# Performance work log

Hardware: AMD Instinct MI355X
Metric: run time of the kernel (lower is better)

## Reference

```python
import jax, jax.numpy as jnp
import numpy as np
from jax import lax

B, D, H, E, TOPK = 4096, 512, 1024, 16, 4


def setup_inputs() -> dict:
    key = jax.random.key(0)
    ks = jax.random.split(key, 7)
    s = 0.02
    return {
        "x": jax.random.normal(ks[0], (B, D), jnp.float32),
        "gate_x": jax.random.normal(ks[1], (B, D), jnp.float32),
        "w_gate": jax.random.normal(ks[2], (D, E), jnp.float32) * s,
        "w1": jax.random.normal(ks[3], (E, D, H), jnp.float32) * s,
        "b1": jax.random.normal(ks[4], (E, H), jnp.float32) * s,
        "w2": jax.random.normal(ks[5], (E, H, D), jnp.float32) * s,
        "b2": jax.random.normal(ks[6], (E, D), jnp.float32) * s,
        "k": TOPK,
    }


def _cv_squared(v):
    # torch .var() is unbiased (ddof=1)
    eps = 1e-10
    return jnp.var(v, ddof=1) / (jnp.mean(v) ** 2 + eps)


def reference(x, gate_x, w_gate, w1, b1, w2, b2, k):
    # --- noisy_top_k_gating with train=False (clean logits path) ---
    logits = gate_x @ w_gate                      # [B, E]
    top_logits, top_idx = lax.top_k(logits, min(k + 1, E))
    topk_logits = top_logits[:, :k]               # [B, k]
    topk_idx = top_idx[:, :k]                     # [B, k]
    topk_gates = jax.nn.softmax(topk_logits, axis=1)
    batch_ar = jnp.arange(logits.shape[0])[:, None]
    gates = jnp.zeros_like(logits).at[batch_ar, topk_idx].set(topk_gates)  # [B, E]

    load = (gates > 0).sum(axis=0).astype(jnp.float32)   # [E]
    importance = gates.sum(axis=0)                        # [E]
    loss = _cv_squared(importance) + _cv_squared(load)

    # --- dispatch / per-expert MLP / weighted combine ---
    # Mathematically identical to SparseDispatcher: output[b] = sum_e gates[b,e]*MLP_e(x[b]).
    # Expressed as a vectorized per-expert GEMM; zero gates null out non-routed experts.
    h = jax.nn.relu(jnp.einsum('bd,edh->ebh', x, w1) + b1[:, None, :])  # [E, B, H]
    expert_out = jnp.einsum('ebh,eho->ebo', h, w2) + b2[:, None, :]      # [E, B, D]
    y = jnp.einsum('be,ebo->bo', gates, expert_out)                      # [B, D]
    return y, loss
```

## Files before the change

kernel.cpp:

```cpp
#include <hip/hip_runtime.h>
#include <cstdint>
#include <cstddef>

#define B_TOK 4096
#define DIM   512
#define HID   1024
#define NEXP  16
#define NSLOT 4

typedef __bf16 bf16x8 __attribute__((ext_vector_type(8)));
typedef float  f32x4  __attribute__((ext_vector_type(4)));
typedef unsigned short ushort8 __attribute__((ext_vector_type(8)));
typedef unsigned short ushort4v __attribute__((ext_vector_type(4)));

static __device__ __forceinline__ unsigned short f2bf(float f) {
    union { float f; unsigned u; } v; v.f = f;
    unsigned r = v.u + 0x7FFFu + ((v.u >> 16) & 1u);
    return (unsigned short)(r >> 16);
}
static __device__ __forceinline__ float bf2f(unsigned short u) {
    union { unsigned u; float f; } v; v.u = (unsigned)u << 16; return v.f;
}

static __device__ __forceinline__ void gl_lds16(const unsigned short* g, unsigned short* l) {
    __builtin_amdgcn_global_load_lds(
        (const __attribute__((address_space(1))) unsigned int*)(const void*)g,
        (__attribute__((address_space(3))) unsigned int*)(void*)l, 16, 0, 0);
}

static __device__ __forceinline__ bf16x8 fragRD(const unsigned short* s, int row, int ks) {
    int byte = row * 128 + ((ks * 2) ^ ((row & 7) << 4));
    return *(const bf16x8*)((const char*)s + byte);
}

#define LOGITS_OFF 0x0000000u
#define LTOK_OFF   0x0100000u
#define LGATE_OFF  0x0140000u
#define CTRL_OFF   0x0180000u
#define PMAP_OFF   0x01A0000u
#define XBF_OFF    0x0200000u
#define W1T_OFF    0x0600000u
#define W2T_OFF    0x1600000u
#define H_OFF      0x2600000u
#define YS_OFF     W1T_OFF

__global__ __launch_bounds__(256) void k_init(
        int* cnt, float* imp,
        const float* __restrict__ x, unsigned short* __restrict__ xbf,
        const float* __restrict__ w1, unsigned short* __restrict__ w1t,
        const float* __restrict__ gx, const float* __restrict__ wg,
        float* __restrict__ logits) {
    __shared__ unsigned short T[64][74];
    const int bid = blockIdx.x;
    const int t = threadIdx.x;
    if (bid < 1024) {
        int row = bid * 4 + (t >> 6);
        int l = t & 63;
        int e = l & 15;
        int c = l >> 4;
        const float* xr = gx + (size_t)row * DIM + c * 128;
        const float* wc = wg + (size_t)(c * 128) * NEXP + e;
        float s = 0.0f;
        #pragma unroll 8
        for (int d = 0; d < 128; d += 4) {
            float4 v = *(const float4*)(xr + d);
            s += v.x * wc[(d + 0) * NEXP] + v.y * wc[(d + 1) * NEXP]
               + v.z * wc[(d + 2) * NEXP] + v.w * wc[(d + 3) * NEXP];
        }
        s += __shfl_xor(s, 16);
        s += __shfl_xor(s, 32);
        if (l < NEXP) logits[row * NEXP + l] = s;
        return;
    }
    if (bid < 2048) {
        int i = (bid - 1024) * 256 + t;
        const float4* s = (const float4*)(x + (size_t)i * 8);
        float4 a = s[0], b = s[1];
        ushort8 v = { f2bf(a.x), f2bf(a.y), f2bf(a.z), f2bf(a.w),
                      f2bf(b.x), f2bf(b.y), f2bf(b.z), f2bf(b.w) };
        *(ushort8*)(xbf + (size_t)i * 8) = v;
        if (bid == 1024 && t < NEXP) { cnt[t] = 0; imp[t] = 0.0f; }
        return;
    }
    const int idx = bid - 2048;
    const int ktiles = DIM >> 6;
    const int e   = idx >> 7;
    const int rem = idx & 127;
    const int k0 = (rem % ktiles) * 64;
    const int n0 = (rem / ktiles) * 64;
    const int kr = t >> 4, n4 = (t & 15) * 4;
    #pragma unroll
    for (int it = 0; it < 4; it++) {
        int k = kr + it * 16;
        float4 v = *(const float4*)(w1 + ((size_t)e * DIM + k0 + k) * HID + n0 + n4);
        T[n4 + 0][k] = f2bf(v.x);
        T[n4 + 1][k] = f2bf(v.y);
        T[n4 + 2][k] = f2bf(v.z);
        T[n4 + 3][k] = f2bf(v.w);
    }
    __syncthreads();
    const int nn = t >> 3, k8 = (t & 7) * 8;
    #pragma unroll
    for (int rep = 0; rep < 2; rep++) {
        int n = nn + rep * 32;
        ushort8 o;
        #pragma unroll
        for (int i = 0; i < 8; i++) o[i] = T[n][k8 + i];
        *(ushort8*)(w1t + ((size_t)e * HID + n0 + n) * DIM + k0 + k8) = o;
    }
}

__global__ __launch_bounds__(256) void k_route(const float* __restrict__ logits,
                        int* __restrict__ cnt, float* __restrict__ imp,
                        int* __restrict__ ltok, float* __restrict__ lgate,
                        int* __restrict__ posmap) {
    __shared__ int   lcnt[NEXP];
    __shared__ float limp[NEXP];
    __shared__ int   lbase[NEXP];
    const int t = threadIdx.x;
    if (t < NEXP) { lcnt[t] = 0; limp[t] = 0.0f; }
    __syncthreads();

    const int b = blockIdx.x * blockDim.x + t;
    float lg[NEXP];
    #pragma unroll
    for (int i = 0; i < NEXP; i++) lg[i] = logits[b * NEXP + i];

    int idx[NSLOT]; float val[NSLOT];
    unsigned used = 0;
    #pragma unroll
    for (int j = 0; j < NSLOT; j++) {
        float bv = -1e30f; int bi = 0;
        #pragma unroll
        for (int i = 0; i < NEXP; i++) {
            bool ok = !((used >> i) & 1u);
            if (ok && lg[i] > bv) { bv = lg[i]; bi = i; }
        }
        idx[j] = bi; val[j] = bv; used |= (1u << bi);
    }
    float m = val[0];
    float ex[NSLOT]; float sum = 0.0f;
    #pragma unroll
    for (int j = 0; j < NSLOT; j++) { ex[j] = __expf(val[j] - m); sum += ex[j]; }
    float inv = 1.0f / sum;

    int   lpos[NSLOT];
    float gv[NSLOT];
    #pragma unroll
    for (int j = 0; j < NSLOT; j++) {
        gv[j] = ex[j] * inv;
        lpos[j] = atomicAdd(&lcnt[idx[j]], 1);
        atomicAdd(&limp[idx[j]], gv[j]);
    }
    __syncthreads();
    if (t < NEXP) {
        lbase[t] = atomicAdd(&cnt[t], lcnt[t]);
        atomicAdd(&imp[t], limp[t]);
    }
    __syncthreads();
    #pragma unroll
    for (int j = 0; j < NSLOT; j++) {
        int e = idx[j];
        int p = lbase[e] + lpos[j];
        ltok[e * B_TOK + p]  = b;
        lgate[e * B_TOK + p] = gv[j];
        posmap[b * NSLOT + j] = (e << 12) | p;
    }
}

__global__ void k_prep(int* __restrict__ ctrl, float* __restrict__ out_loss) {
    const int* cnt = ctrl;
    const float* imp = (const float*)(ctrl + 16);
    int* bases = ctrl + 32;
    int* np    = ctrl + 48;
    int* pairs = ctrl + 64;
    int l = threadIdx.x;
    if (l >= 16) return;
    int base = 0, poff = 0;
    #pragma unroll
    for (int j = 0; j < 16; j++) {
        int cj = cnt[j];
        base += (j < l) ? cj : 0;
        poff += (j < l) ? ((cj + 127) >> 7) : 0;
    }
    bases[l] = base;
    int c = cnt[l];
    int ntile = (c + 127) >> 7;
    for (int i = 0; i < ntile; i++) pairs[poff + i] = (l << 16) | i;
    if (l == 15) *np = poff + ntile;

    float cf = (float)c, im = imp[l];
    float sc = cf, si = im;
    #pragma unroll
    for (int m = 8; m >= 1; m >>= 1) { sc += __shfl_xor(sc, m, 16); si += __shfl_xor(si, m, 16); }
    float ml = sc / 16.0f, mi = si / 16.0f;
    float dc = cf - ml, di = im - mi;
    float vc = dc * dc, vi = di * di;
    #pragma unroll
    for (int m = 8; m >= 1; m >>= 1) { vc += __shfl_xor(vc, m, 16); vi += __shfl_xor(vi, m, 16); }
    vc /= 15.0f; vi /= 15.0f;
    if (l == 0) *out_loss = vi / (mi * mi + 1e-10f) + vc / (ml * ml + 1e-10f);
}

__global__ __launch_bounds__(256, 4) void k_ffn1(
        const unsigned short* __restrict__ xbf, const unsigned short* __restrict__ w1t,
        const float* __restrict__ b1, const int* __restrict__ ctrl,
        const int* __restrict__ ltok, unsigned short* __restrict__ hbuf,
        const float* __restrict__ w2, unsigned short* __restrict__ w2t) {
    __shared__ __align__(16) unsigned short Sh[2][128 * 64];
    __shared__ int toks[128];

    const int orig = blockIdx.x;
    const int tid = threadIdx.x;

    if (orig >= 1280) {
        unsigned short (*T)[74] = (unsigned short (*)[74])&Sh[0][0];
        const int idx = orig - 1280;
        const int ktiles = HID >> 6;
        const int e   = idx >> 7;
        const int rem = idx & 127;
        const int k0 = (rem % ktiles) * 64;
        const int n0 = (rem / ktiles) * 64;
        const int kr = tid >> 4, n4 = (tid & 15) * 4;
        #pragma unroll
        for (int it = 0; it < 4; it++) {
            int k = kr + it * 16;
            float4 v = *(const float4*)(w2 + ((size_t)e * HID + k0 + k) * DIM + n0 + n4);
            T[n4 + 0][k] = f2bf(v.x);
            T[n4 + 1][k] = f2bf(v.y);
            T[n4 + 2][k] = f2bf(v.z);
            T[n4 + 3][k] = f2bf(v.w);
        }
        __syncthreads();
        const int nn = tid >> 3, k8 = (tid & 7) * 8;
        #pragma unroll
        for (int rep = 0; rep < 2; rep++) {
            int n = nn + rep * 32;
            ushort8 o;
            #pragma unroll
            for (int i = 0; i < 8; i++) o[i] = T[n][k8 + i];
            *(ushort8*)(w2t + ((size_t)e * DIM + n0 + n) * HID + k0 + k8) = o;
        }
        return;
    }

    const int wgid = (orig & 7) * 160 + (orig >> 3);
    const int pi = wgid >> 3, nt = wgid & 7;
    if (pi >= ctrl[48]) return;
    const int pr = ctrl[64 + pi];
    const int e  = pr >> 16;
    const int mt = pr & 0xffff;
    const int n_e = ctrl[e];
    const int base = ctrl[32 + e];
    const int row0 = mt * 128;

    unsigned short* As = &Sh[0][0];
    unsigned short* Bs = &Sh[1][0];

    const int lane = tid & 63, wv = tid >> 6;
    const int wm = wv >> 1, wn = wv & 1;
    const int lr = lane & 15, lq = lane >> 4;

    if (tid < 128) toks[tid] = ltok[e * B_TOK + min(row0 + tid, n_e - 1)];
    __syncthreads();

    const unsigned short* a_src[4];
    const unsigned short* b_src[4];
    #pragma unroll
    for (int c = 0; c < 4; c++) {
        int s = (wv * 4 + c) * 64 + lane;
        int r = s >> 3;
        int kc = (s & 7) ^ (r & 7);
        a_src[c] = xbf + (size_t)toks[r] * DIM + kc * 8;
        b_src[c] = w1t + ((size_t)(e * HID + nt * 128 + r)) * DIM + kc * 8;
    }

    f32x4 acc[4][4];
    #pragma unroll
    for (int m = 0; m < 4; m++)
        #pragma unroll
        for (int n = 0; n < 4; n++) acc[m][n] = (f32x4){0.f, 0.f, 0.f, 0.f};

    for (int kt = 0; kt < DIM; kt += 64) {
        #pragma unroll
        for (int c = 0; c < 4; c++) {
            gl_lds16(a_src[c] + kt, &As[(wv * 4 + c) * 512]);
            gl_lds16(b_src[c] + kt, &Bs[(wv * 4 + c) * 512]);
        }
        __syncthreads();
        #pragma unroll
        for (int kk = 0; kk < 64; kk += 32) {
            bf16x8 af[4], bfr[4];
            #pragma unroll
            for (int i = 0; i < 4; i++) {
                af[i]  = fragRD(As, wm * 64 + i * 16 + lr, kk + lq * 8);
                bfr[i] = fragRD(Bs, wn * 64 + i * 16 + lr, kk + lq * 8);
            }
            #pragma unroll
            for (int i = 0; i < 4; i++)
                #pragma unroll
                for (int j = 0; j < 4; j++)
                    acc[i][j] = __builtin_amdgcn_mfma_f32_16x16x32_bf16(af[i], bfr[j], acc[i][j], 0, 0, 0);
        }
        __syncthreads();
    }

    unsigned short* St = &Sh[0][0];
    #pragma unroll
    for (int j = 0; j < 4; j++) {
        int col = wn * 64 + j * 16 + lr;
        float bias = b1[e * HID + nt * 128 + col];
        #pragma unroll
        for (int i = 0; i < 4; i++) {
            #pragma unroll
            for (int q = 0; q < 4; q++) {
                int row = wm * 64 + i * 16 + lq * 4 + q;
                float v = acc[i][j][q] + bias;
                v = v > 0.0f ? v : 0.0f;
                int byte = row * 256 + ((col * 2) ^ ((row & 7) << 4));
                *(unsigned short*)((char*)St + byte) = f2bf(v);
            }
        }
    }
    __syncthreads();
    #pragma unroll
    for (int r8 = 0; r8 < 8; r8++) {
        int idx = r8 * 2048 + tid * 8;
        int row = idx >> 7;
        int colw = idx & 127;
        int pos = row0 + row;
        if (pos < n_e) {
            int byte = row * 256 + ((colw * 2) ^ ((row & 7) << 4));
            ushort8 o = *(const ushort8*)((const char*)St + byte);
            *(ushort8*)(hbuf + (size_t)(base + pos) * HID + nt * 128 + colw) = o;
        }
    }
}

__global__ __launch_bounds__(256, 3) void k_ffn2(
        const unsigned short* __restrict__ hbuf, const unsigned short* __restrict__ w2t,
        const float* __restrict__ b2, const int* __restrict__ ctrl,
        const int* __restrict__ ltok, const float* __restrict__ lgate,
        unsigned short* __restrict__ yslot) {
    const int orig = blockIdx.x;
    const int wgid = (orig & 7) * 72 + (orig >> 3);
    const int pi = wgid >> 2, nt = wgid & 3;
    if (pi >= ctrl[48]) return;
    const int pr = ctrl[64 + pi];
    const int e  = pr >> 16;
    const int mt = pr & 0xffff;
    const int n_e = ctrl[e];
    const int base = ctrl[32 + e];
    const int row0 = mt * 128;

    __shared__ __align__(16) unsigned short Sh[2][128 * 64];
    __shared__ float gts[128];
    unsigned short* As = &Sh[0][0];
    unsigned short* Bs = &Sh[1][0];

    const int tid = threadIdx.x;
    const int lane = tid & 63, wv = tid >> 6;
    const int wm = wv >> 1, wn = wv & 1;
    const int lr = lane & 15, lq = lane >> 4;

    if (tid < 128) {
        int p = min(row0 + tid, n_e - 1);
        gts[tid] = lgate[e * B_TOK + p];
    }
    __syncthreads();

    const unsigned short* a_src[4];
    const unsigned short* b_src[4];
    #pragma unroll
    for (int c = 0; c < 4; c++) {
        int s = (wv * 4 + c) * 64 + lane;
        int r = s >> 3;
        int kc = (s & 7) ^ (r & 7);
        a_src[c] = hbuf + (size_t)(base + min(row0 + r, n_e - 1)) * HID + kc * 8;
        b_src[c] = w2t + ((size_t)(e * DIM + nt * 128 + r)) * HID + kc * 8;
    }

    f32x4 acc[4][4];
    #pragma unroll
    for (int m = 0; m < 4; m++)
        #pragma unroll
        for (int n = 0; n < 4; n++) acc[m][n] = (f32x4){0.f, 0.f, 0.f, 0.f};

    for (int kt = 0; kt < HID; kt += 64) {
        #pragma unroll
        for (int c = 0; c < 4; c++) {
            gl_lds16(a_src[c] + kt, &As[(wv * 4 + c) * 512]);
            gl_lds16(b_src[c] + kt, &Bs[(wv * 4 + c) * 512]);
        }
        __syncthreads();
        #pragma unroll
        for (int kk = 0; kk < 64; kk += 32) {
            bf16x8 af[4], bfr[4];
            #pragma unroll
            for (int i = 0; i < 4; i++) {
                af[i]  = fragRD(As, wm * 64 + i * 16 + lr, kk + lq * 8);
                bfr[i] = fragRD(Bs, wn * 64 + i * 16 + lr, kk + lq * 8);
            }
            #pragma unroll
            for (int i = 0; i < 4; i++)
                #pragma unroll
                for (int j = 0; j < 4; j++)
                    acc[i][j] = __builtin_amdgcn_mfma_f32_16x16x32_bf16(af[i], bfr[j], acc[i][j], 0, 0, 0);
        }
        __syncthreads();
    }

    unsigned short* St = &Sh[0][0];
    #pragma unroll
    for (int j = 0; j < 4; j++) {
        int col = wn * 64 + j * 16 + lr;
        float bias = b2[e * DIM + nt * 128 + col];
        #pragma unroll
        for (int i = 0; i < 4; i++) {
            #pragma unroll
            for (int q = 0; q < 4; q++) {
                int row = wm * 64 + i * 16 + lq * 4 + q;
                float v = (acc[i][j][q] + bias) * gts[row];
                int byte = row * 256 + ((col * 2) ^ ((row & 7) << 4));
                *(unsigned short*)((char*)St + byte) = f2bf(v);
            }
        }
    }
    __syncthreads();
    #pragma unroll
    for (int r8 = 0; r8 < 8; r8++) {
        int idx = r8 * 2048 + tid * 8;
        int row = idx >> 7;
        int colw = idx & 127;
        int pos = row0 + row;
        if (pos < n_e) {
            int byte = row * 256 + ((colw * 2) ^ ((row & 7) << 4));
            ushort8 o = *(const ushort8*)((const char*)St + byte);
            *(ushort8*)(yslot + (size_t)(base + pos) * DIM + nt * 128 + colw) = o;
        }
    }
}

__global__ __launch_bounds__(256) void k_gather(
        const unsigned short* __restrict__ yslot, const int* __restrict__ posmap,
        const int* __restrict__ ctrl, float* __restrict__ y) {
    const int tok = blockIdx.x * 2 + (threadIdx.x >> 7);
    const int c4  = (threadIdx.x & 127) * 4;
    float4 s = {0.f, 0.f, 0.f, 0.f};
    #pragma unroll
    for (int j = 0; j < NSLOT; j++) {
        int pm = posmap[tok * NSLOT + j];
        int e = pm >> 12, p = pm & 4095;
        size_t row = (size_t)(ctrl[32 + e] + p);
        ushort4v v = *(const ushort4v*)(yslot + row * DIM + c4);
        s.x += bf2f(v[0]); s.y += bf2f(v[1]); s.z += bf2f(v[2]); s.w += bf2f(v[3]);
    }
    *(float4*)(y + (size_t)tok * DIM + c4) = s;
}

extern "C" void kernel_launch(void* const* d_in, const int* in_sizes, int n_in,
                              void* d_out, int out_size, void* d_ws, size_t ws_size,
                              hipStream_t stream) {
    const float* x  = (const float*)d_in[0];
    const float* gx = (const float*)d_in[1];
    const float* wg = (const float*)d_in[2];
    const float* w1 = (const float*)d_in[3];
    const float* b1 = (const float*)d_in[4];
    const float* w2 = (const float*)d_in[5];
    const float* b2 = (const float*)d_in[6];
    float* out = (float*)d_out;

    char* ws = (char*)d_ws;
    float* logits = (float*)(ws + LOGITS_OFF);
    int*   ltok   = (int*)(ws + LTOK_OFF);
    float* lgate  = (float*)(ws + LGATE_OFF);
    int*   ctrl   = (int*)(ws + CTRL_OFF);
    int*   cnt    = ctrl;
    float* imp    = (float*)(ctrl + 16);
    int*   posmap = (int*)(ws + PMAP_OFF);
    unsigned short* xbf   = (unsigned short*)(ws + XBF_OFF);
    unsigned short* w1t   = (unsigned short*)(ws + W1T_OFF);
    unsigned short* w2t   = (unsigned short*)(ws + W2T_OFF);
    unsigned short* hbuf  = (unsigned short*)(ws + H_OFF);
    unsigned short* yslot = (unsigned short*)(ws + YS_OFF);

    hipLaunchKernelGGL(k_init, dim3(4096), dim3(256), 0, stream,
                       cnt, imp, x, xbf, w1, w1t, gx, wg, logits);
    hipLaunchKernelGGL(k_route, dim3(B_TOK / 256), dim3(256), 0, stream,
                       logits, cnt, imp, ltok, lgate, posmap);
    hipLaunchKernelGGL(k_prep, dim3(1), dim3(64), 0, stream, ctrl,
                       out + (size_t)B_TOK * DIM);
    hipLaunchKernelGGL(k_ffn1, dim3(3328), dim3(256), 0, stream,
                       xbf, w1t, b1, ctrl, ltok, hbuf, w2, w2t);
    hipLaunchKernelGGL(k_ffn2, dim3(576), dim3(256), 0, stream,
                       hbuf, w2t, b2, ctrl, ltok, lgate, yslot);
    hipLaunchKernelGGL(k_gather, dim3(B_TOK / 2), dim3(256), 0, stream,
                       yslot, posmap, ctrl, out);
}
```

Baseline: 96.66 us.

## Widen ffn1 tiles to 128x256 and pack per-tile descriptors

The first expert GEMM now computes 128x256 output tiles per workgroup instead of 128x128, halving the number of GEMM workgroups and reusing each loaded A tile across twice as many columns. This raises accumulator registers (launch bounds drop to 2 waves/SIMD), grows LDS to 48KB, and the epilogue is done in two halves with extra barriers. k_prep also writes a packed int4 descriptor (expert, tile, count, base) per tile so both FFN kernels fetch routing metadata in one load instead of several dependent ones.

```diff
diff --git a/kernel.cpp b/kernel.cpp
--- a/kernel.cpp
+++ b/kernel.cpp
@@ -186,7 +186,11 @@
     bases[l] = base;
     int c = cnt[l];
     int ntile = (c + 127) >> 7;
-    for (int i = 0; i < ntile; i++) pairs[poff + i] = (l << 16) | i;
+    for (int i = 0; i < ntile; i++) {
+        pairs[poff + i] = (l << 16) | i;
+        int4* d = (int4*)(ctrl + 256 + (poff + i) * 4);
+        *d = make_int4(l, i, c, base);
+    }
     if (l == 15) *np = poff + ntile;
 
     float cf = (float)c, im = imp[l];
@@ -202,20 +206,20 @@
     if (l == 0) *out_loss = vi / (mi * mi + 1e-10f) + vc / (ml * ml + 1e-10f);
 }
 
-__global__ __launch_bounds__(256, 4) void k_ffn1(
+__global__ __launch_bounds__(256, 2) void k_ffn1(
         const unsigned short* __restrict__ xbf, const unsigned short* __restrict__ w1t,
         const float* __restrict__ b1, const int* __restrict__ ctrl,
         const int* __restrict__ ltok, unsigned short* __restrict__ hbuf,
         const float* __restrict__ w2, unsigned short* __restrict__ w2t) {
-    __shared__ __align__(16) unsigned short Sh[2][128 * 64];
+    __shared__ __align__(16) unsigned short Sh[3 * 8192];
     __shared__ int toks[128];
 
     const int orig = blockIdx.x;
     const int tid = threadIdx.x;
 
-    if (orig >= 1280) {
-        unsigned short (*T)[74] = (unsigned short (*)[74])&Sh[0][0];
-        const int idx = orig - 1280;
+    if (orig >= 576) {
+        unsigned short (*T)[74] = (unsigned short (*)[74])&Sh[0];
+        const int idx = orig - 576;
         const int ktiles = HID >> 6;
         const int e   = idx >> 7;
         const int rem = idx & 127;
@@ -244,18 +248,17 @@
         return;
     }
 
-    const int wgid = (orig & 7) * 160 + (orig >> 3);
-    const int pi = wgid >> 3, nt = wgid & 7;
+    const int wgid = (orig & 7) * 72 + (orig >> 3);
+    const int pi = wgid >> 2, nt = wgid & 3;
     if (pi >= ctrl[48]) return;
-    const int pr = ctrl[64 + pi];
-    const int e  = pr >> 16;
-    const int mt = pr & 0xffff;
-    const int n_e = ctrl[e];
-    const int base = ctrl[32 + e];
-    const int row0 = mt * 128;
-
-    unsigned short* As = &Sh[0][0];
-    unsigned short* Bs = &Sh[1][0];
+    const int4 dsc = *(const int4*)(ctrl + 256 + pi * 4);
+    const int e   = dsc.x;
+    const int n_e = dsc.z;
+    const int base = dsc.w;
+    const int row0 = dsc.y * 128;
+
+    unsigned short* As = &Sh[0];
+    unsigned short* Bs = &Sh[8192];
 
     const int lane = tid & 63, wv = tid >> 6;
     const int wm = wv >> 1, wn = wv & 1;
@@ -265,75 +268,88 @@
     __syncthreads();
 
     const unsigned short* a_src[4];
-    const unsigned short* b_src[4];
+    const unsigned short* b_src[8];
     #pragma unroll
     for (int c = 0; c < 4; c++) {
         int s = (wv * 4 + c) * 64 + lane;
         int r = s >> 3;
         int kc = (s & 7) ^ (r & 7);
         a_src[c] = xbf + (size_t)toks[r] * DIM + kc * 8;
-        b_src[c] = w1t + ((size_t)(e * HID + nt * 128 + r)) * DIM + kc * 8;
-    }
-
-    f32x4 acc[4][4];
+    }
+    #pragma unroll
+    for (int c = 0; c < 8; c++) {
+        int s = (wv * 8 + c) * 64 + lane;
+        int r = s >> 3;
+        int kc = (s & 7) ^ (r & 7);
+        b_src[c] = w1t + ((size_t)(e * HID + nt * 256 + r)) * DIM + kc * 8;
+    }
+
+    f32x4 acc[4][8];
     #pragma unroll
     for (int m = 0; m < 4; m++)
         #pragma unroll
-        for (int n = 0; n < 4; n++) acc[m][n] = (f32x4){0.f, 0.f, 0.f, 0.f};
+        for (int n = 0; n < 8; n++) acc[m][n] = (f32x4){0.f, 0.f, 0.f, 0.f};
 
     for (int kt = 0; kt < DIM; kt += 64) {
         #pragma unroll
-        for (int c = 0; c < 4; c++) {
-            gl_lds16(a_src[c] + kt, &As[(wv * 4 + c) * 512]);
-            gl_lds16(b_src[c] + kt, &Bs[(wv * 4 + c) * 512]);
-        }
+        for (int c = 0; c < 4; c++) gl_lds16(a_src[c] + kt, &As[(wv * 4 + c) * 512]);
+        #pragma unroll
+        for (int c = 0; c < 8; c++) gl_lds16(b_src[c] + kt, &Bs[(wv * 8 + c) * 512]);
         __syncthreads();
         #pragma unroll
         for (int kk = 0; kk < 64; kk += 32) {
-            bf16x8 af[4], bfr[4];
-            #pragma unroll
-            for (int i = 0; i < 4; i++) {
-                af[i]  = fragRD(As, wm * 64 + i * 16 + lr, kk + lq * 8);
-                bfr[i] = fragRD(Bs, wn * 64 + i * 16 + lr, kk + lq * 8);
-            }
-            #pragma unroll
-            for (int i = 0; i < 4; i++)
+            bf16x8 af[4];
+            #pragma unroll
+            for (int i = 0; i < 4; i++) af[i] = fragRD(As, wm * 64 + i * 16 + lr, kk + lq * 8);
+            #pragma unroll
+            for (int h = 0; h < 2; h++) {
+                bf16x8 bfr[4];
                 #pragma unroll
                 for (int j = 0; j < 4; j++)
-                    acc[i][j] = __builtin_amdgcn_mfma_f32_16x16x32_bf16(af[i], bfr[j], acc[i][j], 0, 0, 0);
-        }
-        __syncthreads();
-    }
-
-    unsigned short* St = &Sh[0][0];
-    #pragma unroll
-    for (int j = 0; j < 4; j++) {
-        int col = wn * 64 + j * 16 + lr;
-        float bias = b1[e * HID + nt * 128 + col];
-        #pragma unroll
-        for (int i = 0; i < 4; i++) {
-            #pragma unroll
-            for (int q = 0; q < 4; q++) {
-                int row = wm * 64 + i * 16 + lq * 4 + q;
-                float v = acc[i][j][q] + bias;
-                v = v > 0.0f ? v : 0.0f;
-                int byte = row * 256 + ((col * 2) ^ ((row & 7) << 4));
-                *(unsigned short*)((char*)St + byte) = f2bf(v);
+                    bfr[j] = fragRD(Bs, h * 128 + wn * 64 + j * 16 + lr, kk + lq * 8);
+                #pragma unroll
+                for (int i = 0; i < 4; i++)
+                    #pragma unroll
+                    for (int j = 0; j < 4; j++)
+                        acc[i][h * 4 + j] = __builtin_amdgcn_mfma_f32_16x16x32_bf16(af[i], bfr[j], acc[i][h * 4 + j], 0, 0, 0);
             }
         }
-    }
-    __syncthreads();
-    #pragma unroll
-    for (int r8 = 0; r8 < 8; r8++) {
-        int idx = r8 * 2048 + tid * 8;
-        int row = idx >> 7;
-        int colw = idx & 127;
-        int pos = row0 + row;
-        if (pos < n_e) {
-            int byte = row * 256 + ((colw * 2) ^ ((row & 7) << 4));
-            ushort8 o = *(const ushort8*)((const char*)St + byte);
-            *(ushort8*)(hbuf + (size_t)(base + pos) * HID + nt * 128 + colw) = o;
-        }
+        __syncthreads();
+    }
+
+    unsigned short* St = &Sh[0];
+    #pragma unroll
+    for (int h = 0; h < 2; h++) {
+        #pragma unroll
+        for (int j = 0; j < 4; j++) {
+            int col = wn * 64 + j * 16 + lr;
+            float bias = b1[e * HID + nt * 256 + h * 128 + col];
+            #pragma unroll
+            for (int i = 0; i < 4; i++) {
+                #pragma unroll
+                for (int q = 0; q < 4; q++) {
+                    int row = wm * 64 + i * 16 + lq * 4 + q;
+                    float v = acc[i][h * 4 + j][q] + bias;
+                    v = v > 0.0f ? v : 0.0f;
+                    int byte = row * 256 + ((col * 2) ^ ((row & 7) << 4));
+                    *(unsigned short*)((char*)St + byte) = f2bf(v);
+                }
+            }
+        }
+        __syncthreads();
+        #pragma unroll
+        for (int r8 = 0; r8 < 8; r8++) {
+            int idx = r8 * 2048 + tid * 8;
+            int row = idx >> 7;
+            int colw = idx & 127;
+            int pos = row0 + row;
+            if (pos < n_e) {
+                int byte = row * 256 + ((colw * 2) ^ ((row & 7) << 4));
+                ushort8 o = *(const ushort8*)((const char*)St + byte);
+                *(ushort8*)(hbuf + (size_t)(base + pos) * HID + nt * 256 + h * 128 + colw) = o;
+            }
+        }
+        __syncthreads();
     }
 }
 
@@ -346,12 +362,11 @@
     const int wgid = (orig & 7) * 72 + (orig >> 3);
     const int pi = wgid >> 2, nt = wgid & 3;
     if (pi >= ctrl[48]) return;
-    const int pr = ctrl[64 + pi];
-    const int e  = pr >> 16;
-    const int mt = pr & 0xffff;
-    const int n_e = ctrl[e];
-    const int base = ctrl[32 + e];
-    const int row0 = mt * 128;
+    const int4 dsc = *(const int4*)(ctrl + 256 + pi * 4);
+    const int e   = dsc.x;
+    const int n_e = dsc.z;
+    const int base = dsc.w;
+    const int row0 = dsc.y * 128;
 
     __shared__ __align__(16) unsigned short Sh[2][128 * 64];
     __shared__ float gts[128];
@@ -490,7 +505,7 @@
                        logits, cnt, imp, ltok, lgate, posmap);
     hipLaunchKernelGGL(k_prep, dim3(1), dim3(64), 0, stream, ctrl,
                        out + (size_t)B_TOK * DIM);
-    hipLaunchKernelGGL(k_ffn1, dim3(3328), dim3(256), 0, stream,
+    hipLaunchKernelGGL(k_ffn1, dim3(2624), dim3(256), 0, stream,
                        xbf, w1t, b1, ctrl, ltok, hbuf, w2, w2t);
     hipLaunchKernelGGL(k_ffn2, dim3(576), dim3(256), 0, stream,
                        hbuf, w2t, b2, ctrl, ltok, lgate, yslot);
```

New measurement: 98.43 us. No clear change (+1.8%).

## Double-buffer LDS tiles in both expert GEMMs and pack tile descriptors

Applied to the files above, without the earlier changes.

Both expert GEMM kernels now prefetch the next K-slice of A and B into a second LDS buffer while MFMAs run on the current one. This removes the per-iteration load-then-barrier stall and cuts one barrier per K step. The prep kernel also writes a packed int4 descriptor (expert, tile, count, base) per work item, so each GEMM block reads its metadata with one load instead of several dependent ones. LDS per block doubles to 64KB and launch bounds drop to 2 blocks/CU, which lowers occupancy. The descriptor array at ctrl+256 assumes the control buffer is large enough.

```diff
diff --git a/kernel.cpp b/kernel.cpp
--- a/kernel.cpp
+++ b/kernel.cpp
@@ -186,7 +186,11 @@
     bases[l] = base;
     int c = cnt[l];
     int ntile = (c + 127) >> 7;
-    for (int i = 0; i < ntile; i++) pairs[poff + i] = (l << 16) | i;
+    for (int i = 0; i < ntile; i++) {
+        pairs[poff + i] = (l << 16) | i;
+        int4* d = (int4*)(ctrl + 256 + (poff + i) * 4);
+        *d = make_int4(l, i, c, base);
+    }
     if (l == 15) *np = poff + ntile;
 
     float cf = (float)c, im = imp[l];
@@ -202,12 +206,12 @@
     if (l == 0) *out_loss = vi / (mi * mi + 1e-10f) + vc / (ml * ml + 1e-10f);
 }
 
-__global__ __launch_bounds__(256, 4) void k_ffn1(
+__global__ __launch_bounds__(256, 2) void k_ffn1(
         const unsigned short* __restrict__ xbf, const unsigned short* __restrict__ w1t,
         const float* __restrict__ b1, const int* __restrict__ ctrl,
         const int* __restrict__ ltok, unsigned short* __restrict__ hbuf,
         const float* __restrict__ w2, unsigned short* __restrict__ w2t) {
-    __shared__ __align__(16) unsigned short Sh[2][128 * 64];
+    __shared__ __align__(16) unsigned short Sh[2][16384];
     __shared__ int toks[128];
 
     const int orig = blockIdx.x;
@@ -247,15 +251,11 @@
     const int wgid = (orig & 7) * 160 + (orig >> 3);
     const int pi = wgid >> 3, nt = wgid & 7;
     if (pi >= ctrl[48]) return;
-    const int pr = ctrl[64 + pi];
-    const int e  = pr >> 16;
-    const int mt = pr & 0xffff;
-    const int n_e = ctrl[e];
-    const int base = ctrl[32 + e];
-    const int row0 = mt * 128;
-
-    unsigned short* As = &Sh[0][0];
-    unsigned short* Bs = &Sh[1][0];
+    const int4 dsc = *(const int4*)(ctrl + 256 + pi * 4);
+    const int e   = dsc.x;
+    const int n_e = dsc.z;
+    const int base = dsc.w;
+    const int row0 = dsc.y * 128;
 
     const int lane = tid & 63, wv = tid >> 6;
     const int wm = wv >> 1, wn = wv & 1;
@@ -281,13 +281,24 @@
         #pragma unroll
         for (int n = 0; n < 4; n++) acc[m][n] = (f32x4){0.f, 0.f, 0.f, 0.f};
 
+    #pragma unroll
+    for (int c = 0; c < 4; c++) {
+        gl_lds16(a_src[c], &Sh[0][(wv * 4 + c) * 512]);
+        gl_lds16(b_src[c], &Sh[0][8192 + (wv * 4 + c) * 512]);
+    }
+    __syncthreads();
+
+    int p = 0;
     for (int kt = 0; kt < DIM; kt += 64) {
-        #pragma unroll
-        for (int c = 0; c < 4; c++) {
-            gl_lds16(a_src[c] + kt, &As[(wv * 4 + c) * 512]);
-            gl_lds16(b_src[c] + kt, &Bs[(wv * 4 + c) * 512]);
-        }
-        __syncthreads();
+        if (kt + 64 < DIM) {
+            #pragma unroll
+            for (int c = 0; c < 4; c++) {
+                gl_lds16(a_src[c] + kt + 64, &Sh[p ^ 1][(wv * 4 + c) * 512]);
+                gl_lds16(b_src[c] + kt + 64, &Sh[p ^ 1][8192 + (wv * 4 + c) * 512]);
+            }
+        }
+        const unsigned short* As = &Sh[p][0];
+        const unsigned short* Bs = &Sh[p][8192];
         #pragma unroll
         for (int kk = 0; kk < 64; kk += 32) {
             bf16x8 af[4], bfr[4];
@@ -303,6 +314,7 @@
                     acc[i][j] = __builtin_amdgcn_mfma_f32_16x16x32_bf16(af[i], bfr[j], acc[i][j], 0, 0, 0);
         }
         __syncthreads();
+        p ^= 1;
     }
 
     unsigned short* St = &Sh[0][0];
@@ -337,7 +349,7 @@
     }
 }
 
-__global__ __launch_bounds__(256, 3) void k_ffn2(
+__global__ __launch_bounds__(256, 2) void k_ffn2(
         const unsigned short* __restrict__ hbuf, const unsigned short* __restrict__ w2t,
         const float* __restrict__ b2, const int* __restrict__ ctrl,
         const int* __restrict__ ltok, const float* __restrict__ lgate,
@@ -346,17 +358,14 @@
     const int wgid = (orig & 7) * 72 + (orig >> 3);
     const int pi = wgid >> 2, nt = wgid & 3;
     if (pi >= ctrl[48]) return;
-    const int pr = ctrl[64 + pi];
-    const int e  = pr >> 16;
-    const int mt = pr & 0xffff;
-    const int n_e = ctrl[e];
-    const int base = ctrl[32 + e];
-    const int row0 = mt * 128;
-
-    __shared__ __align__(16) unsigned short Sh[2][128 * 64];
+    const int4 dsc = *(const int4*)(ctrl + 256 + pi * 4);
+    const int e   = dsc.x;
+    const int n_e = dsc.z;
+    const int base = dsc.w;
+    const int row0 = dsc.y * 128;
+
+    __shared__ __align__(16) unsigned short Sh[2][16384];
     __shared__ float gts[128];
-    unsigned short* As = &Sh[0][0];
-    unsigned short* Bs = &Sh[1][0];
 
     const int tid = threadIdx.x;
     const int lane = tid & 63, wv = tid >> 6;
@@ -386,13 +395,24 @@
         #pragma unroll
         for (int n = 0; n < 4; n++) acc[m][n] = (f32x4){0.f, 0.f, 0.f, 0.f};
 
+    #pragma unroll
+    for (int c = 0; c < 4; c++) {
+        gl_lds16(a_src[c], &Sh[0][(wv * 4 + c) * 512]);
+        gl_lds16(b_src[c], &Sh[0][8192 + (wv * 4 + c) * 512]);
+    }
+    __syncthreads();
+
+    int p = 0;
     for (int kt = 0; kt < HID; kt += 64) {
-        #pragma unroll
-        for (int c = 0; c < 4; c++) {
-            gl_lds16(a_src[c] + kt, &As[(wv * 4 + c) * 512]);
-            gl_lds16(b_src[c] + kt, &Bs[(wv * 4 + c) * 512]);
-        }
-        __syncthreads();
+        if (kt + 64 < HID) {
+            #pragma unroll
+            for (int c = 0; c < 4; c++) {
+                gl_lds16(a_src[c] + kt + 64, &Sh[p ^ 1][(wv * 4 + c) * 512]);
+                gl_lds16(b_src[c] + kt + 64, &Sh[p ^ 1][8192 + (wv * 4 + c) * 512]);
+            }
+        }
+        const unsigned short* As = &Sh[p][0];
+        const unsigned short* Bs = &Sh[p][8192];
         #pragma unroll
         for (int kk = 0; kk < 64; kk += 32) {
             bf16x8 af[4], bfr[4];
@@ -408,6 +428,7 @@
                     acc[i][j] = __builtin_amdgcn_mfma_f32_16x16x32_bf16(af[i], bfr[j], acc[i][j], 0, 0, 0);
         }
         __syncthreads();
+        p ^= 1;
     }
 
     unsigned short* St = &Sh[0][0];
```

New measurement: 106.0 us. 9.7% more time.
